# Kernel tuning notes

Measured on AMD Instinct MI355X. Metric: run time of the kernel, lower is better.

## Reference

```python
import jax, jax.numpy as jnp
from jax import lax
import numpy as np

D = 8        # domain_num
L = 12       # label_num
C = 9        # attr_num
W = 128      # window_size
B = 4096
EPS = 1e-5


def setup_inputs() -> dict:
    key = jax.random.key(0)
    ks = jax.random.split(key, 12)
    s = 0.05
    return {
        "x": jax.random.normal(ks[0], (B, C, 1, W), dtype=jnp.float32),
        "weights": jax.random.uniform(ks[1], (B, D), dtype=jnp.float32),
        # per-domain stacked parameters (leading dim D)
        "gamma": jnp.ones((D, C), dtype=jnp.float32),
        "beta": jnp.zeros((D, C), dtype=jnp.float32),
        "w1": jax.random.normal(ks[2], (D, 32, C, 9), dtype=jnp.float32) * s,
        "b1": jax.random.normal(ks[3], (D, 32), dtype=jnp.float32) * s,
        "w2": jax.random.normal(ks[4], (D, 64, 32, 9), dtype=jnp.float32) * s,
        "b2": jax.random.normal(ks[5], (D, 64), dtype=jnp.float32) * s,
        "fcw": jax.random.normal(ks[6], (D, L, 64 * 26), dtype=jnp.float32) * s,
        "fcb": jax.random.normal(ks[7], (D, L), dtype=jnp.float32) * s,
    }


def _maxpool2(h):
    # MaxPool along width, kernel 2 stride 2 (height is 1 and already squeezed)
    b, c, w = h.shape
    return h.reshape(b, c, w // 2, 2).max(axis=-1)


def _branch(x3, gamma, beta, w1, b1, w2, b2, fcw, fcb):
    # x3: [B, C, W]. BatchNorm2d in training mode: batch stats over (N, H, W).
    mean = x3.mean(axis=(0, 2), keepdims=True)
    var = x3.var(axis=(0, 2), keepdims=True)
    xn = (x3 - mean) * lax.rsqrt(var + EPS) * gamma[None, :, None] + beta[None, :, None]
    dn = ('NCH', 'OIH', 'NCH')
    h = lax.conv_general_dilated(xn, w1, (1,), 'VALID', dimension_numbers=dn)
    h = _maxpool2(jax.nn.relu(h + b1[None, :, None]))          # [B,32,60]
    h = lax.conv_general_dilated(h, w2, (1,), 'VALID', dimension_numbers=dn)
    h = _maxpool2(jax.nn.relu(h + b2[None, :, None]))          # [B,64,26]
    flat = h.reshape(h.shape[0], 64 * 26)
    return jax.nn.relu(flat @ fcw.T + fcb)                      # [B,L]


def reference(x, weights, gamma, beta, w1, b1, w2, b2, fcw, fcb):
    x3 = x[:, :, 0, :]  # squeeze height=1 -> [B,C,W]
    per_domain = jax.vmap(_branch, in_axes=(None, 0, 0, 0, 0, 0, 0, 0, 0))(
        x3, gamma, beta, w1, b1, w2, b2, fcw, fcb)              # [D,B,L]
    # vectorized form of the nested python-loop weighted sum over domains
    return jnp.einsum('bd,dbl->bl', weights, per_domain)        # [B,L]
```

## Files before the change

### kernel.cpp

```cpp
#include <hip/hip_runtime.h>
#include <hip/hip_bf16.h>

#define D 8
#define L 12
#define C 9
#define W 128
#define B 4096
#define EPS 1e-5f

typedef __attribute__((ext_vector_type(8))) short v8s;
typedef __attribute__((ext_vector_type(4))) float v4f;

#define OFF_STATS 0
#define OFF_B1E   1152
#define OFF_W1T   1408
#define OFF_W2T   21888
#define OFF_FCWP  95616

__device__ inline unsigned short f2bf(float f) {
    unsigned u = __builtin_bit_cast(unsigned, f);
    u += 0x7FFFu + ((u >> 16) & 1u);
    return (unsigned short)(u >> 16);
}
__device__ inline unsigned pk2(float a, float b) {
    float2 f2; f2.x = a; f2.y = b;
    __hip_bfloat162 h = __float22bfloat162_rn(f2);
    unsigned u; __builtin_memcpy(&u, &h, 4);
    return u;
}

__global__ void stats_repack_kernel(const float* __restrict__ x,
                                    const float* __restrict__ w2,
                                    const float* __restrict__ fcw,
                                    float* __restrict__ ws) {
    const int t = threadIdx.x;
    __shared__ float redS[8];
    if (blockIdx.x < 576) {
        const int c = blockIdx.x % 9;
        const int slice = blockIdx.x / 9;
        const int w4 = t & 31, br = t >> 5;
        const float4* x4 = (const float4*)x;
        float s = 0.f, s2 = 0.f;
        for (int b = slice * 8 + br; b < B; b += 64 * 8) {
            float4 v = x4[(size_t)b * 288 + c * 32 + w4];
            s  += v.x + v.y + v.z + v.w;
            s2 += v.x * v.x + v.y * v.y + v.z * v.z + v.w * v.w;
        }
        for (int off = 32; off >= 1; off >>= 1) {
            s  += __shfl_down(s, off);
            s2 += __shfl_down(s2, off);
        }
        if ((t & 63) == 0) { redS[(t >> 6) * 2] = s; redS[(t >> 6) * 2 + 1] = s2; }
        __syncthreads();
        if (t == 0) {
            ws[OFF_STATS + slice * 18 + c]     = redS[0] + redS[2] + redS[4] + redS[6];
            ws[OFF_STATS + slice * 18 + 9 + c] = redS[1] + redS[3] + redS[5] + redS[7];
        }
    } else {
        const int i0 = blockIdx.x - 576;
        const int d = i0 / 5, part = i0 % 5;
        short* w2t  = (short*)(ws + OFF_W2T);
        short* fcwp = (short*)(ws + OFF_FCWP);
        if (part < 2) {
            for (int i = part * 256 + t; i < 64 * 9 * 32; i += 512) {
                int o = i / 288, r = i % 288, tap = r / 32, ic = r & 31;
                w2t[(size_t)d * 18432 + i] =
                    (short)f2bf(w2[(((size_t)(d * 64 + o)) * 32 + ic) * 9 + tap]);
            }
        } else {
            for (int i = (part - 2) * 256 + t; i < 12 * 1664; i += 768) {
                int l = i / 1664, k = i % 1664, p = k >> 6, o = k & 63;
                fcwp[((size_t)d * 12) * 1664 + i] =
                    (short)f2bf(fcw[((size_t)(d * 12 + l)) * 1664 + o * 26 + p]);
            }
        }
    }
}

__global__ void fold1_kernel(const float* __restrict__ w1, const float* __restrict__ b1,
                             const float* __restrict__ gamma, const float* __restrict__ beta,
                             float* __restrict__ ws) {
    const int d = blockIdx.x, t = threadIdx.x;
    __shared__ float g[9], bt[9];
    if (t < 64) {
        for (int c = 0; c < 9; c++) {
            float s  = ws[OFF_STATS + t * 18 + c];
            float s2 = ws[OFF_STATS + t * 18 + 9 + c];
            for (int off = 32; off >= 1; off >>= 1) {
                s  += __shfl_down(s, off);
                s2 += __shfl_down(s2, off);
            }
            if (t == 0) {
                const float N = (float)B * (float)W;
                float m  = s / N;
                float vv = s2 / N - m * m;
                float inv = rsqrtf(vv + EPS);
                float gg = gamma[d * 9 + c] * inv;
                g[c] = gg; bt[c] = beta[d * 9 + c] - gg * m;
            }
        }
    }
    __syncthreads();
    const int o = t >> 3, sub = t & 7;
    short* w1t = (short*)(ws + OFF_W1T);
    short* dst = w1t + (size_t)d * 5120 + o * 160;
    const float* src = w1 + ((size_t)(d * 32 + o)) * 81;
    float bias_part = 0.f;
    for (int tap = sub; tap < 10; tap += 8) {
        for (int c = 0; c < 16; c++) {
            float v = 0.f;
            if (tap < 9 && c < 9) {
                float wv = src[c * 9 + tap];
                v = wv * g[c];
                bias_part += wv * bt[c];
            }
            dst[tap * 16 + c] = (short)f2bf(v);
        }
    }
    bias_part += __shfl_xor(bias_part, 1);
    bias_part += __shfl_xor(bias_part, 2);
    bias_part += __shfl_xor(bias_part, 4);
    if (sub == 0) ws[OFF_B1E + d * 32 + o] = b1[d * 32 + o] + bias_part;
}

__global__ __launch_bounds__(256, 4)
void branch_kernel(const float* __restrict__ x,
                   const float* __restrict__ b2g,
                   const float* __restrict__ fcb,
                   const float* __restrict__ wts,
                   const float* __restrict__ ws,
                   float* __restrict__ out) {
    const int t = threadIdx.x;
    const int lane = t & 63;
    const int wv = t >> 6;
    const int d = blockIdx.y;
    const int b0 = blockIdx.x * 4;
    const short* w1t  = (const short*)(ws + OFF_W1T) + (size_t)d * 5120;
    const short* w2t  = (const short*)(ws + OFF_W2T) + (size_t)d * 18432;
    const short* fcwp = (const short*)(ws + OFF_FCWP) + (size_t)d * 12 * 1664;
    const float* b1e  = ws + OFF_B1E + d * 32;

    __shared__ __align__(16) short lds[9216];
    short* myr = &lds[wv * 2304];

    const int n = lane & 15, quad = lane >> 4;

    {
        const float* xrow = x + (size_t)(b0 + wv) * 1152;
        #pragma unroll
        for (int rep = 0; rep < 2; rep++) {
            const int w = lane + rep * 64;
            float v[9];
            #pragma unroll
            for (int c = 0; c < 9; c++) v[c] = xrow[c * 128 + w];
            uint4 lo, hi;
            lo.x = pk2(v[0], v[1]); lo.y = pk2(v[2], v[3]);
            lo.z = pk2(v[4], v[5]); lo.w = pk2(v[6], v[7]);
            hi.x = (unsigned)(unsigned short)f2bf(v[8]); hi.y = 0; hi.z = 0; hi.w = 0;
            *(uint4*)&myr[(0 * 144 + w) * 8] = lo;
            *(uint4*)&myr[(1 * 144 + w) * 8] = hi;
        }
        if (lane < 16) {
            uint4 z; z.x = z.y = z.z = z.w = 0;
            *(uint4*)&myr[(0 * 144 + 128 + lane) * 8] = z;
            *(uint4*)&myr[(1 * 144 + 128 + lane) * 8] = z;
        }
    }

    {
        const int qh = quad >> 1, ql = quad & 1;
        const float bias0 = b1e[n], bias1 = b1e[16 + n];
        v4f acc[8][2];
        #pragma unroll
        for (int mt = 0; mt < 8; mt++)
            #pragma unroll
            for (int nt = 0; nt < 2; nt++) { v4f z = {0.f,0.f,0.f,0.f}; acc[mt][nt] = z; }
        #pragma unroll
        for (int s = 0; s < 5; s++) {
            v8s Bw0 = *(const v8s*)&w1t[n * 160 + (2 * s + qh) * 16 + ql * 8];
            v8s Bw1 = *(const v8s*)&w1t[(16 + n) * 160 + (2 * s + qh) * 16 + ql * 8];
            #pragma unroll
            for (int mt = 0; mt < 8; mt++) {
                const int row = mt * 16 + n + 2 * s + qh;
                v8s Af = *(const v8s*)&myr[(ql * 144 + row) * 8];
                acc[mt][0] = __builtin_amdgcn_mfma_f32_16x16x32_bf16(Af, Bw0, acc[mt][0], 0, 0, 0);
                acc[mt][1] = __builtin_amdgcn_mfma_f32_16x16x32_bf16(Af, Bw1, acc[mt][1], 0, 0, 0);
            }
        }
        unsigned held[16];
        #pragma unroll
        for (int mt = 0; mt < 8; mt++)
            #pragma unroll
            for (int nt = 0; nt < 2; nt++) {
                const float bb = nt ? bias1 : bias0;
                float h0  = fmaxf(fmaxf(acc[mt][nt][0], acc[mt][nt][1]) + bb, 0.f);
                float h1v = fmaxf(fmaxf(acc[mt][nt][2], acc[mt][nt][3]) + bb, 0.f);
                held[mt * 2 + nt] = pk2(h0, h1v);
            }
        #pragma unroll
        for (int mt = 0; mt < 8; mt++) {
            const int p = mt * 8 + quad * 2;
            #pragma unroll
            for (int nt = 0; nt < 2; nt++) {
                const unsigned pr = held[mt * 2 + nt];
                const int plane = nt * 2 + (n >> 3);
                const int col = n & 7;
                if (p < 60)     myr[(plane * 72 + p) * 8 + col]     = (short)(pr & 0xFFFFu);
                if (p + 1 < 60) myr[(plane * 72 + p + 1) * 8 + col] = (short)(pr >> 16);
            }
        }
    }

    {
        float biasv[4];
        #pragma unroll
        for (int nt = 0; nt < 4; nt++) biasv[nt] = b2g[d * 64 + nt * 16 + n];
        v4f acc[4][4];
        #pragma unroll
        for (int mt = 0; mt < 4; mt++)
            #pragma unroll
            for (int nt = 0; nt < 4; nt++) { v4f z = {0.f,0.f,0.f,0.f}; acc[mt][nt] = z; }
        for (int tap = 0; tap < 9; tap++) {
            v8s Bw[4];
            #pragma unroll
            for (int nt = 0; nt < 4; nt++)
                Bw[nt] = *(const v8s*)&w2t[(nt * 16 + n) * 288 + tap * 32 + quad * 8];
            #pragma unroll
            for (int mt = 0; mt < 4; mt++) {
                const int row = mt * 16 + n + tap;
                v8s Af = *(const v8s*)&myr[(quad * 72 + row) * 8];
                #pragma unroll
                for (int nt = 0; nt < 4; nt++)
                    acc[mt][nt] = __builtin_amdgcn_mfma_f32_16x16x32_bf16(Af, Bw[nt], acc[mt][nt], 0, 0, 0);
            }
        }
        unsigned held[16];
        #pragma unroll
        for (int mt = 0; mt < 4; mt++)
            #pragma unroll
            for (int nt = 0; nt < 4; nt++) {
                float h0  = fmaxf(fmaxf(acc[mt][nt][0], acc[mt][nt][1]) + biasv[nt], 0.f);
                float h1v = fmaxf(fmaxf(acc[mt][nt][2], acc[mt][nt][3]) + biasv[nt], 0.f);
                held[mt * 4 + nt] = pk2(h0, h1v);
            }
        #pragma unroll
        for (int mt = 0; mt < 4; mt++) {
            const int p = mt * 8 + quad * 2;
            #pragma unroll
            for (int nt = 0; nt < 4; nt++) {
                const unsigned pr = held[mt * 4 + nt];
                const int oc = nt * 16 + n;
                if (p < 26) {
                    const int gs = (oc >> 3) ^ (p & 7);
                    myr[p * 64 + gs * 8 + (oc & 7)] = (short)(pr & 0xFFFFu);
                }
                if (p + 1 < 26) {
                    const int gs = (oc >> 3) ^ ((p + 1) & 7);
                    myr[(p + 1) * 64 + gs * 8 + (oc & 7)] = (short)(pr >> 16);
                }
            }
        }
    }
    __syncthreads();

    {
        const int lrow = (n < 12) ? n : 0;
        v4f acc = {0.f, 0.f, 0.f, 0.f};
        for (int ks = wv; ks < 52; ks += 4) {
            const int p = ks >> 1;
            const int gs = ((ks & 1) * 4 + quad) ^ (p & 7);
            v8s A  = *(const v8s*)&fcwp[lrow * 1664 + ks * 32 + quad * 8];
            v8s Bf = *(const v8s*)&lds[(n & 3) * 2304 + p * 64 + gs * 8];
            acc = __builtin_amdgcn_mfma_f32_16x16x32_bf16(A, Bf, acc, 0, 0, 0);
        }
        float* red = (float*)(myr + 1672);
        *(float4*)&red[lane * 4] = *(float4*)&acc;
    }
    __syncthreads();
    if (t < 64) {
        float sum[4] = {0.f, 0.f, 0.f, 0.f};
        #pragma unroll
        for (int w = 0; w < 4; w++) {
            const float* redw = (const float*)(&lds[w * 2304 + 1672]);
            float4 v = *(const float4*)&redw[lane * 4];
            sum[0] += v.x; sum[1] += v.y; sum[2] += v.z; sum[3] += v.w;
        }
        if (n < 4) {
            const float wgt = wts[(size_t)(b0 + n) * 8 + d];
            #pragma unroll
            for (int r = 0; r < 4; r++) {
                const int l = quad * 4 + r;
                if (l < 12) {
                    float v = fmaxf(sum[r] + fcb[d * 12 + l], 0.f);
                    atomicAdd(&out[(size_t)(b0 + n) * 12 + l], wgt * v);
                }
            }
        }
    }
}

extern "C" void kernel_launch(void* const* d_in, const int* in_sizes, int n_in,
                              void* d_out, int out_size, void* d_ws, size_t ws_size,
                              hipStream_t stream) {
    const float* x       = (const float*)d_in[0];
    const float* weights = (const float*)d_in[1];
    const float* gamma   = (const float*)d_in[2];
    const float* beta    = (const float*)d_in[3];
    const float* w1      = (const float*)d_in[4];
    const float* b1      = (const float*)d_in[5];
    const float* w2      = (const float*)d_in[6];
    const float* b2      = (const float*)d_in[7];
    const float* fcw     = (const float*)d_in[8];
    const float* fcb     = (const float*)d_in[9];
    float* ws  = (float*)d_ws;
    float* out = (float*)d_out;

    (void)hipMemsetAsync(out, 0, (size_t)out_size * sizeof(float), stream);
    stats_repack_kernel<<<dim3(616), 256, 0, stream>>>(x, w2, fcw, ws);
    fold1_kernel<<<dim3(D), 256, 0, stream>>>(w1, b1, gamma, beta, ws);
    branch_kernel<<<dim3(B / 4, D), 256, 0, stream>>>(x, b2, fcb, weights, ws, out);
}
```

Before: 235.5 us.

## Loop over domains inside branch kernel to reuse staged input tile

The domain grid dimension is replaced by an in-kernel loop over all eight domains, so each block loads and converts its four input rows to bf16 in LDS once instead of once per domain. The LDS layout is split into separate regions so the staged input survives across domains, with h1 padded to a 73-row stride. This cuts global reads of x and the conversion work by a factor of eight, but the grid shrinks eightfold to 1024 blocks and each block now runs serially through domains with extra barriers per iteration, which lowers available parallelism and latency hiding.

```diff
diff --git a/kernel.cpp b/kernel.cpp
--- a/kernel.cpp
+++ b/kernel.cpp
@@ -16,6 +16,12 @@
 #define OFF_W1T   1408
 #define OFF_W2T   21888
 #define OFF_FCWP  95616
+
+#define REGION  4640
+#define XB_OFF  0
+#define H1_OFF  2304
+#define H2_OFF  2304
+#define RED_OFF 3976
 
 __device__ inline unsigned short f2bf(float f) {
     unsigned u = __builtin_bit_cast(unsigned, f);
@@ -133,15 +139,10 @@
     const int t = threadIdx.x;
     const int lane = t & 63;
     const int wv = t >> 6;
-    const int d = blockIdx.y;
     const int b0 = blockIdx.x * 4;
-    const short* w1t  = (const short*)(ws + OFF_W1T) + (size_t)d * 5120;
-    const short* w2t  = (const short*)(ws + OFF_W2T) + (size_t)d * 18432;
-    const short* fcwp = (const short*)(ws + OFF_FCWP) + (size_t)d * 12 * 1664;
-    const float* b1e  = ws + OFF_B1E + d * 32;
-
-    __shared__ __align__(16) short lds[9216];
-    short* myr = &lds[wv * 2304];
+
+    __shared__ __align__(16) short lds[4 * REGION];
+    short* myr = &lds[wv * REGION];
 
     const int n = lane & 15, quad = lane >> 4;
 
@@ -157,145 +158,153 @@
             lo.x = pk2(v[0], v[1]); lo.y = pk2(v[2], v[3]);
             lo.z = pk2(v[4], v[5]); lo.w = pk2(v[6], v[7]);
             hi.x = (unsigned)(unsigned short)f2bf(v[8]); hi.y = 0; hi.z = 0; hi.w = 0;
-            *(uint4*)&myr[(0 * 144 + w) * 8] = lo;
-            *(uint4*)&myr[(1 * 144 + w) * 8] = hi;
+            *(uint4*)&myr[XB_OFF + (0 * 144 + w) * 8] = lo;
+            *(uint4*)&myr[XB_OFF + (1 * 144 + w) * 8] = hi;
         }
         if (lane < 16) {
             uint4 z; z.x = z.y = z.z = z.w = 0;
-            *(uint4*)&myr[(0 * 144 + 128 + lane) * 8] = z;
-            *(uint4*)&myr[(1 * 144 + 128 + lane) * 8] = z;
-        }
-    }
-
-    {
-        const int qh = quad >> 1, ql = quad & 1;
-        const float bias0 = b1e[n], bias1 = b1e[16 + n];
-        v4f acc[8][2];
-        #pragma unroll
-        for (int mt = 0; mt < 8; mt++)
-            #pragma unroll
-            for (int nt = 0; nt < 2; nt++) { v4f z = {0.f,0.f,0.f,0.f}; acc[mt][nt] = z; }
-        #pragma unroll
-        for (int s = 0; s < 5; s++) {
-            v8s Bw0 = *(const v8s*)&w1t[n * 160 + (2 * s + qh) * 16 + ql * 8];
-            v8s Bw1 = *(const v8s*)&w1t[(16 + n) * 160 + (2 * s + qh) * 16 + ql * 8];
+            *(uint4*)&myr[XB_OFF + (0 * 144 + 128 + lane) * 8] = z;
+            *(uint4*)&myr[XB_OFF + (1 * 144 + 128 + lane) * 8] = z;
+        }
+    }
+
+    for (int d = 0; d < D; d++) {
+        const short* w1t  = (const short*)(ws + OFF_W1T) + (size_t)d * 5120;
+        const short* w2t  = (const short*)(ws + OFF_W2T) + (size_t)d * 18432;
+        const short* fcwp = (const short*)(ws + OFF_FCWP) + (size_t)d * 12 * 1664;
+        const float* b1e  = ws + OFF_B1E + d * 32;
+
+        {
+            const int qh = quad >> 1, ql = quad & 1;
+            const float bias0 = b1e[n], bias1 = b1e[16 + n];
+            v4f acc[8][2];
+            #pragma unroll
+            for (int mt = 0; mt < 8; mt++)
+                #pragma unroll
+                for (int nt = 0; nt < 2; nt++) { v4f z = {0.f,0.f,0.f,0.f}; acc[mt][nt] = z; }
+            #pragma unroll
+            for (int s = 0; s < 5; s++) {
+                v8s Bw0 = *(const v8s*)&w1t[n * 160 + (2 * s + qh) * 16 + ql * 8];
+                v8s Bw1 = *(const v8s*)&w1t[(16 + n) * 160 + (2 * s + qh) * 16 + ql * 8];
+                #pragma unroll
+                for (int mt = 0; mt < 8; mt++) {
+                    const int row = mt * 16 + n + 2 * s + qh;
+                    v8s Af = *(const v8s*)&myr[XB_OFF + (ql * 144 + row) * 8];
+                    acc[mt][0] = __builtin_amdgcn_mfma_f32_16x16x32_bf16(Af, Bw0, acc[mt][0], 0, 0, 0);
+                    acc[mt][1] = __builtin_amdgcn_mfma_f32_16x16x32_bf16(Af, Bw1, acc[mt][1], 0, 0, 0);
+                }
+            }
+            unsigned held[16];
+            #pragma unroll
+            for (int mt = 0; mt < 8; mt++)
+                #pragma unroll
+                for (int nt = 0; nt < 2; nt++) {
+                    const float bb = nt ? bias1 : bias0;
+                    float h0  = fmaxf(fmaxf(acc[mt][nt][0], acc[mt][nt][1]) + bb, 0.f);
+                    float h1v = fmaxf(fmaxf(acc[mt][nt][2], acc[mt][nt][3]) + bb, 0.f);
+                    held[mt * 2 + nt] = pk2(h0, h1v);
+                }
             #pragma unroll
             for (int mt = 0; mt < 8; mt++) {
-                const int row = mt * 16 + n + 2 * s + qh;
-                v8s Af = *(const v8s*)&myr[(ql * 144 + row) * 8];
-                acc[mt][0] = __builtin_amdgcn_mfma_f32_16x16x32_bf16(Af, Bw0, acc[mt][0], 0, 0, 0);
-                acc[mt][1] = __builtin_amdgcn_mfma_f32_16x16x32_bf16(Af, Bw1, acc[mt][1], 0, 0, 0);
-            }
-        }
-        unsigned held[16];
-        #pragma unroll
-        for (int mt = 0; mt < 8; mt++)
-            #pragma unroll
-            for (int nt = 0; nt < 2; nt++) {
-                const float bb = nt ? bias1 : bias0;
-                float h0  = fmaxf(fmaxf(acc[mt][nt][0], acc[mt][nt][1]) + bb, 0.f);
-                float h1v = fmaxf(fmaxf(acc[mt][nt][2], acc[mt][nt][3]) + bb, 0.f);
-                held[mt * 2 + nt] = pk2(h0, h1v);
-            }
-        #pragma unroll
-        for (int mt = 0; mt < 8; mt++) {
-            const int p = mt * 8 + quad * 2;
-            #pragma unroll
-            for (int nt = 0; nt < 2; nt++) {
-                const unsigned pr = held[mt * 2 + nt];
-                const int plane = nt * 2 + (n >> 3);
-                const int col = n & 7;
-                if (p < 60)     myr[(plane * 72 + p) * 8 + col]     = (short)(pr & 0xFFFFu);
-                if (p + 1 < 60) myr[(plane * 72 + p + 1) * 8 + col] = (short)(pr >> 16);
-            }
-        }
-    }
-
-    {
-        float biasv[4];
-        #pragma unroll
-        for (int nt = 0; nt < 4; nt++) biasv[nt] = b2g[d * 64 + nt * 16 + n];
-        v4f acc[4][4];
-        #pragma unroll
-        for (int mt = 0; mt < 4; mt++)
-            #pragma unroll
-            for (int nt = 0; nt < 4; nt++) { v4f z = {0.f,0.f,0.f,0.f}; acc[mt][nt] = z; }
-        for (int tap = 0; tap < 9; tap++) {
-            v8s Bw[4];
-            #pragma unroll
-            for (int nt = 0; nt < 4; nt++)
-                Bw[nt] = *(const v8s*)&w2t[(nt * 16 + n) * 288 + tap * 32 + quad * 8];
+                const int p = mt * 8 + quad * 2;
+                #pragma unroll
+                for (int nt = 0; nt < 2; nt++) {
+                    const unsigned pr = held[mt * 2 + nt];
+                    const int plane = nt * 2 + (n >> 3);
+                    const int col = n & 7;
+                    if (p < 60)     myr[H1_OFF + (plane * 73 + p) * 8 + col]     = (short)(pr & 0xFFFFu);
+                    if (p + 1 < 60) myr[H1_OFF + (plane * 73 + p + 1) * 8 + col] = (short)(pr >> 16);
+                }
+            }
+        }
+
+        {
+            float biasv[4];
+            #pragma unroll
+            for (int nt = 0; nt < 4; nt++) biasv[nt] = b2g[d * 64 + nt * 16 + n];
+            v4f acc[4][4];
+            #pragma unroll
+            for (int mt = 0; mt < 4; mt++)
+                #pragma unroll
+                for (int nt = 0; nt < 4; nt++) { v4f z = {0.f,0.f,0.f,0.f}; acc[mt][nt] = z; }
+            for (int tap = 0; tap < 9; tap++) {
+                v8s Bw[4];
+                #pragma unroll
+                for (int nt = 0; nt < 4; nt++)
+                    Bw[nt] = *(const v8s*)&w2t[(nt * 16 + n) * 288 + tap * 32 + quad * 8];
+                #pragma unroll
+                for (int mt = 0; mt < 4; mt++) {
+                    const int row = mt * 16 + n + tap;
+                    v8s Af = *(const v8s*)&myr[H1_OFF + (quad * 73 + row) * 8];
+                    #pragma unroll
+                    for (int nt = 0; nt < 4; nt++)
+                        acc[mt][nt] = __builtin_amdgcn_mfma_f32_16x16x32_bf16(Af, Bw[nt], acc[mt][nt], 0, 0, 0);
+                }
+            }
+            unsigned held[16];
+            #pragma unroll
+            for (int mt = 0; mt < 4; mt++)
+                #pragma unroll
+                for (int nt = 0; nt < 4; nt++) {
+                    float h0  = fmaxf(fmaxf(acc[mt][nt][0], acc[mt][nt][1]) + biasv[nt], 0.f);
+                    float h1v = fmaxf(fmaxf(acc[mt][nt][2], acc[mt][nt][3]) + biasv[nt], 0.f);
+                    held[mt * 4 + nt] = pk2(h0, h1v);
+                }
             #pragma unroll
             for (int mt = 0; mt < 4; mt++) {
-                const int row = mt * 16 + n + tap;
-                v8s Af = *(const v8s*)&myr[(quad * 72 + row) * 8];
-                #pragma unroll
-                for (int nt = 0; nt < 4; nt++)
-                    acc[mt][nt] = __builtin_amdgcn_mfma_f32_16x16x32_bf16(Af, Bw[nt], acc[mt][nt], 0, 0, 0);
-            }
-        }
-        unsigned held[16];
-        #pragma unroll
-        for (int mt = 0; mt < 4; mt++)
-            #pragma unroll
-            for (int nt = 0; nt < 4; nt++) {
-                float h0  = fmaxf(fmaxf(acc[mt][nt][0], acc[mt][nt][1]) + biasv[nt], 0.f);
-                float h1v = fmaxf(fmaxf(acc[mt][nt][2], acc[mt][nt][3]) + biasv[nt], 0.f);
-                held[mt * 4 + nt] = pk2(h0, h1v);
-            }
-        #pragma unroll
-        for (int mt = 0; mt < 4; mt++) {
-            const int p = mt * 8 + quad * 2;
-            #pragma unroll
-            for (int nt = 0; nt < 4; nt++) {
-                const unsigned pr = held[mt * 4 + nt];
-                const int oc = nt * 16 + n;
-                if (p < 26) {
-                    const int gs = (oc >> 3) ^ (p & 7);
-                    myr[p * 64 + gs * 8 + (oc & 7)] = (short)(pr & 0xFFFFu);
-                }
-                if (p + 1 < 26) {
-                    const int gs = (oc >> 3) ^ ((p + 1) & 7);
-                    myr[(p + 1) * 64 + gs * 8 + (oc & 7)] = (short)(pr >> 16);
-                }
-            }
-        }
-    }
-    __syncthreads();
-
-    {
-        const int lrow = (n < 12) ? n : 0;
-        v4f acc = {0.f, 0.f, 0.f, 0.f};
-        for (int ks = wv; ks < 52; ks += 4) {
-            const int p = ks >> 1;
-            const int gs = ((ks & 1) * 4 + quad) ^ (p & 7);
-            v8s A  = *(const v8s*)&fcwp[lrow * 1664 + ks * 32 + quad * 8];
-            v8s Bf = *(const v8s*)&lds[(n & 3) * 2304 + p * 64 + gs * 8];
-            acc = __builtin_amdgcn_mfma_f32_16x16x32_bf16(A, Bf, acc, 0, 0, 0);
-        }
-        float* red = (float*)(myr + 1672);
-        *(float4*)&red[lane * 4] = *(float4*)&acc;
-    }
-    __syncthreads();
-    if (t < 64) {
-        float sum[4] = {0.f, 0.f, 0.f, 0.f};
-        #pragma unroll
-        for (int w = 0; w < 4; w++) {
-            const float* redw = (const float*)(&lds[w * 2304 + 1672]);
-            float4 v = *(const float4*)&redw[lane * 4];
-            sum[0] += v.x; sum[1] += v.y; sum[2] += v.z; sum[3] += v.w;
-        }
-        if (n < 4) {
-            const float wgt = wts[(size_t)(b0 + n) * 8 + d];
-            #pragma unroll
-            for (int r = 0; r < 4; r++) {
-                const int l = quad * 4 + r;
-                if (l < 12) {
-                    float v = fmaxf(sum[r] + fcb[d * 12 + l], 0.f);
-                    atomicAdd(&out[(size_t)(b0 + n) * 12 + l], wgt * v);
-                }
-            }
-        }
+                const int p = mt * 8 + quad * 2;
+                #pragma unroll
+                for (int nt = 0; nt < 4; nt++) {
+                    const unsigned pr = held[mt * 4 + nt];
+                    const int oc = nt * 16 + n;
+                    if (p < 26) {
+                        const int gs = (oc >> 3) ^ (p & 7);
+                        myr[H2_OFF + p * 64 + gs * 8 + (oc & 7)] = (short)(pr & 0xFFFFu);
+                    }
+                    if (p + 1 < 26) {
+                        const int gs = (oc >> 3) ^ ((p + 1) & 7);
+                        myr[H2_OFF + (p + 1) * 64 + gs * 8 + (oc & 7)] = (short)(pr >> 16);
+                    }
+                }
+            }
+        }
+        __syncthreads();
+
+        {
+            const int lrow = (n < 12) ? n : 0;
+            v4f acc = {0.f, 0.f, 0.f, 0.f};
+            for (int ks = wv; ks < 52; ks += 4) {
+                const int p = ks >> 1;
+                const int gs = ((ks & 1) * 4 + quad) ^ (p & 7);
+                v8s A  = *(const v8s*)&fcwp[lrow * 1664 + ks * 32 + quad * 8];
+                v8s Bf = *(const v8s*)&lds[(n & 3) * REGION + H2_OFF + p * 64 + gs * 8];
+                acc = __builtin_amdgcn_mfma_f32_16x16x32_bf16(A, Bf, acc, 0, 0, 0);
+            }
+            float* red = (float*)(myr + RED_OFF);
+            *(float4*)&red[lane * 4] = *(float4*)&acc;
+        }
+        __syncthreads();
+        if (t < 64) {
+            float sum[4] = {0.f, 0.f, 0.f, 0.f};
+            #pragma unroll
+            for (int w = 0; w < 4; w++) {
+                const float* redw = (const float*)(&lds[w * REGION + RED_OFF]);
+                float4 v = *(const float4*)&redw[lane * 4];
+                sum[0] += v.x; sum[1] += v.y; sum[2] += v.z; sum[3] += v.w;
+            }
+            if (n < 4) {
+                const float wgt = wts[(size_t)(b0 + n) * 8 + d];
+                #pragma unroll
+                for (int r = 0; r < 4; r++) {
+                    const int l = quad * 4 + r;
+                    if (l < 12) {
+                        float v = fmaxf(sum[r] + fcb[d * 12 + l], 0.f);
+                        atomicAdd(&out[(size_t)(b0 + n) * 12 + l], wgt * v);
+                    }
+                }
+            }
+        }
+        __syncthreads();
     }
 }
 
@@ -318,5 +327,5 @@
     (void)hipMemsetAsync(out, 0, (size_t)out_size * sizeof(float), stream);
     stats_repack_kernel<<<dim3(616), 256, 0, stream>>>(x, w2, fcw, ws);
     fold1_kernel<<<dim3(D), 256, 0, stream>>>(w1, b1, gamma, beta, ws);
-    branch_kernel<<<dim3(B / 4, D), 256, 0, stream>>>(x, b2, fcb, weights, ws, out);
-}
+    branch_kernel<<<dim3(B / 4), 256, 0, stream>>>(x, b2, fcb, weights, ws, out);
+}
```

New measurement: 333.7 us. 41.7% more time.
